# Performance work log

Hardware: AMD Instinct MI355X
Metric: run time of the kernel (lower is better)

## Reference

```python
import jax, jax.numpy as jnp
import numpy as np

SR = 3            # search_range
K = 5             # template_sz
S = 2 * SR + 1    # search window size (7)
KSZ = 5           # bilateral kernel size
SIG_S = 1.5       # bilateral spatial sigma
SIG_I = 0.05      # bilateral intensity sigma


def _patches(x, k, pad):
    # x: (B,C,H,W) -> (B, C*k*k, H', W'); channel order (C, kh, kw) matches torch unfold
    return jax.lax.conv_general_dilated_patches(x, (k, k), (1, 1), pad)


def _binomial(x):
    # separable [1 2 1]/4 with replicate padding
    xp = jnp.pad(x, ((0, 0), (0, 0), (1, 1), (0, 0)), mode='edge')
    v = (xp[:, :, :-2, :] + 2.0 * x + xp[:, :, 2:, :]) / 4.0
    vp = jnp.pad(v, ((0, 0), (0, 0), (0, 0), (1, 1)), mode='edge')
    return (vp[:, :, :, :-2] + 2.0 * v + vp[:, :, :, 2:]) / 4.0


def _gradient(f):
    fp = jnp.pad(f, ((0, 0), (0, 0), (1, 1), (1, 1)), mode='edge')
    fy = (fp[:, :, 2:, 1:-1] - fp[:, :, :-2, 1:-1]) / 2.0
    fx = (fp[:, :, 1:-1, 2:] - fp[:, :, 1:-1, :-2]) / 2.0
    return fy, fx


def _templates(img):
    # (B,1,H,W) -> (B,H,W,1,K*K)  per-pixel KxK patch (zero SAME padding)
    p = _patches(img, K, [(K // 2, K // 2)] * 2)      # (B,K*K,H,W)
    return jnp.transpose(p, (0, 2, 3, 1))[:, :, :, None, :]


def _search_windows(img):
    # (B,1,H,W) -> (B,H,W,S*S,K*K): KxK templates at every displacement in SxS window
    B, _, H, W = img.shape
    xp = jnp.pad(img, ((0, 0), (0, 0), (SR, SR), (SR, SR)))      # zero pad by max_sr
    p1 = _patches(xp, K, [(K // 2, K // 2)] * 2)                  # (B,K*K,H+2SR,W+2SR)
    p2 = _patches(p1, S, 'VALID')                                 # (B,K*K*S*S,H,W)
    p2 = p2.reshape(B, K * K, S, S, H, W)
    return jnp.transpose(p2, (0, 4, 5, 2, 3, 1)).reshape(B, H, W, S * S, K * K)


def _spiral_rank():
    # rank of each flat (S*S) displacement in a center-out spiral traversal
    sz = S
    order = np.zeros(sz * sz, np.int32)
    j = i = 0
    rank = 0
    order[(j + SR) * sz + (i + SR)] = rank
    rank += 1
    dirs = [(0, 1), (1, 0), (0, -1), (-1, 0)]
    d, step = 0, 1
    while rank < sz * sz:
        for _ in range(2):
            dj, di = dirs[d % 4]
            for _ in range(step):
                j += dj
                i += di
                if abs(j) <= SR and abs(i) <= SR and rank < sz * sz:
                    order[(j + SR) * sz + (i + SR)] = rank
                    rank += 1
            d += 1
        step += 1
    return jnp.asarray(order)


def _subpixel(f_t, g_t, f_img):
    # f_t, g_t: (B,H,W,1,K*K) in 0..255; f_img: (B,1,H,W) float in [0,1]
    f = f_t / 255.0
    g = g_t / 255.0
    dfy_img, dfx_img = _gradient(f_img)
    dfy = _templates(dfy_img)
    dfx = _templates(dfx_img)
    pm = np.zeros((K, K), np.float32)
    pm[0, :] = pm[-1, :] = pm[:, 0] = pm[:, -1] = 1.0   # border ring mask
    pred = jnp.asarray(pm.reshape(-1))
    rs = lambda x: jnp.sum(x, axis=-1, keepdims=True)
    a = rs(dfx * dfx * pred)
    b = rs(dfx * dfy * pred)
    d = rs(dfy * dfy * pred)
    z = g - f
    p = rs(z * dfx * pred)
    q = rs(z * dfy * pred)
    det = a * d - b * b
    u = d * p - b * q
    v = a * q - b * p
    sub = jnp.concatenate([v, u], axis=-1)              # (B,H,W,1,2) (y,x)
    det_bad = det <= 1e-7
    sub = sub / jnp.where(det_bad, 1.0, det)            # safe divide; masked anyway
    sub = jnp.where(det_bad | (jnp.abs(sub) >= 1.0), 0.0, sub)
    return jnp.transpose(sub[:, :, :, 0, :], (0, 3, 1, 2))   # (B,2,H,W)


def _median3(x):
    # 3x3 median with replicate (SYMMETRIC) padding
    B, C, H, W = x.shape
    xp = jnp.pad(x, ((0, 0), (0, 0), (1, 1), (1, 1)), mode='edge')
    p = _patches(xp, 3, 'VALID').reshape(B, C, 9, H, W)
    return jnp.sort(p, axis=2)[:, :, 4]


def _bilateral(t, vec):
    # t: (B,1,H,W) guide; vec: (B,2,H,W) flow
    B, _, H, W = t.shape
    k2 = KSZ * KSZ
    kernel = -1.0 / (2.0 * SIG_S ** 2) * jnp.ones((k2,), jnp.float32)
    sii = 1.0 / (2.0 * SIG_I ** 2)
    cp = jnp.transpose(t, (0, 2, 3, 1))[:, :, :, None, :]                # (B,H,W,1,1)
    ck = jnp.transpose(_patches(t, KSZ, [(KSZ // 2, KSZ // 2)] * 2).reshape(B, 1, k2, H, W), (0, 3, 4, 2, 1))  # (B,H,W,k2,1)
    idiff = jnp.sum((cp - ck) ** 2, axis=-1)                             # (B,H,W,k2)
    coeff = jnp.clip(1.0 - jnp.abs(kernel - idiff * sii), 0.0, 1.0)[..., None]
    vb = jnp.transpose(_patches(vec, KSZ, [(KSZ // 2, KSZ // 2)] * 2).reshape(B, 2, k2, H, W), (0, 3, 4, 2, 1))  # (B,H,W,k2,2)
    out = jnp.sum(vb * coeff, axis=-2) / jnp.sum(coeff, axis=-2)
    return jnp.transpose(out, (0, 3, 1, 2))


def setup_inputs() -> dict:
    key = jax.random.key(0)
    k1, k2 = jax.random.split(key)
    H = W = 256
    f_img = jax.random.uniform(k1, (1, 1, H, W), jnp.float32)
    g_img = jax.random.uniform(k2, (1, 1, H, W), jnp.float32)
    return {'f_img': f_img, 'g_img': g_img}


def reference(f_img, g_img):
    fb = _binomial(f_img)
    gb = _binomial(g_img)
    # quantize to uint8-valued floats (matches _cast float->uint8)
    fq = jnp.clip(jnp.round(fb * 255.0), 0.0, 255.0)
    gq = jnp.clip(jnp.round(gb * 255.0), 0.0, 255.0)
    w1 = _search_windows(fq)                 # (B,H,W,S*S,K*K)
    w2 = _templates(gq)                      # (B,H,W,1,K*K)
    cost = jnp.sum(jnp.abs(w1 - w2), axis=-1).astype(jnp.int32)   # (B,H,W,S*S)
    rank = _spiral_rank()
    score = cost * 64 + rank                 # lexicographic (cost, spiral rank); rank < 64
    idx = jnp.argmin(score, axis=-1)         # (B,H,W) spiral-centered argmin
    rng = jnp.arange(-SR, SR + 1, dtype=jnp.float32)
    jj, ii = jnp.meshgrid(rng, rng, indexing='ij')
    vecLUT = -jnp.stack([jj, ii], axis=-1).reshape(-1, 2)
    vector = jnp.transpose(vecLUT[idx], (0, 3, 1, 2))             # (B,2,H,W)
    min_t = jnp.take_along_axis(w1, idx[:, :, :, None, None], axis=3)  # (B,H,W,1,K*K)
    sub = _subpixel(min_t, w2, fb)
    flow = vector + sub
    flow = _median3(flow)
    flow = _bilateral(fb, flow)
    return flow
```

## Files before the change

kernel.cpp:

```cpp
#include <hip/hip_runtime.h>
#include <math.h>

#define H 256
#define W 256
#define TS 16

#if __has_builtin(__builtin_amdgcn_alignbyte)
__device__ __forceinline__ unsigned align_b(unsigned hi, unsigned lo, int sh) {
    return __builtin_amdgcn_alignbyte(hi, lo, sh);
}
#else
__device__ __forceinline__ unsigned align_b(unsigned hi, unsigned lo, int sh) {
    unsigned d;
    asm("v_alignbyte_b32 %0, %1, %2, %3" : "=v"(d) : "v"(hi), "v"(lo), "v"(sh));
    return d;
}
#endif

#if __has_builtin(__builtin_amdgcn_sad_u8)
__device__ __forceinline__ unsigned sad_u8(unsigned a, unsigned b, unsigned acc) {
    return __builtin_amdgcn_sad_u8(a, b, acc);
}
#else
__device__ __forceinline__ unsigned sad_u8(unsigned a, unsigned b, unsigned acc) {
    unsigned d;
    asm("v_sad_u8 %0, %1, %2, %3" : "=v"(d) : "v"(a), "v"(b), "v"(acc));
    return d;
}
#endif

__global__ void k_binq(const float* __restrict__ f, const float* __restrict__ g,
                       float* __restrict__ fb,
                       unsigned char* __restrict__ fq, unsigned char* __restrict__ gq) {
    int x = blockIdx.x * blockDim.x + threadIdx.x;
    int y = blockIdx.y * blockDim.y + threadIdx.y;
    if (x >= W || y >= H) return;
    int ym = max(y - 1, 0), yp = min(y + 1, H - 1);
    int xm = max(x - 1, 0), xp = min(x + 1, W - 1);

    float fvm = (f[ym*W+xm] + 2.0f*f[y*W+xm] + f[yp*W+xm]) * 0.25f;
    float fv0 = (f[ym*W+x ] + 2.0f*f[y*W+x ] + f[yp*W+x ]) * 0.25f;
    float fvp = (f[ym*W+xp] + 2.0f*f[y*W+xp] + f[yp*W+xp]) * 0.25f;
    float fbv = (fvm + 2.0f*fv0 + fvp) * 0.25f;

    float gvm = (g[ym*W+xm] + 2.0f*g[y*W+xm] + g[yp*W+xm]) * 0.25f;
    float gv0 = (g[ym*W+x ] + 2.0f*g[y*W+x ] + g[yp*W+x ]) * 0.25f;
    float gvp = (g[ym*W+xp] + 2.0f*g[y*W+xp] + g[yp*W+xp]) * 0.25f;
    float gbv = (gvm + 2.0f*gv0 + gvp) * 0.25f;

    fb[y*W+x] = fbv;
    fq[y*W+x] = (unsigned char)fminf(fmaxf(rintf(fbv * 255.0f), 0.0f), 255.0f);
    gq[y*W+x] = (unsigned char)fminf(fmaxf(rintf(gbv * 255.0f), 0.0f), 255.0f);
}

__global__ void __launch_bounds__(256)
k_search(const unsigned char* __restrict__ fq, const unsigned char* __restrict__ gq,
         const float* __restrict__ fb, float* __restrict__ flow) {
    __shared__ unsigned sfq[26 * 7];
    __shared__ unsigned sgq[20 * 5];
    __shared__ float    sfb[22 * 22];

    int tx = threadIdx.x, ty = threadIdx.y;
    int bx0 = blockIdx.x * TS, by0 = blockIdx.y * TS;
    int tid = ty * TS + tx;

    unsigned char* sfq_b = (unsigned char*)sfq;
    unsigned char* sgq_b = (unsigned char*)sgq;

    for (int i = tid; i < 26 * 28; i += 256) {
        int r = i / 28, c = i % 28;
        int gy = by0 + r - 5, gx = bx0 + c - 5;
        sfq_b[i] = (gy >= 0 && gy < H && gx >= 0 && gx < W) ? fq[gy*W+gx] : 0;
    }
    for (int i = tid; i < 20 * 20; i += 256) {
        int r = i / 20, c = i % 20;
        int gy = by0 + r - 2, gx = bx0 + c - 2;
        sgq_b[r * 20 + c] = (gy >= 0 && gy < H && gx >= 0 && gx < W) ? gq[gy*W+gx] : 0;
    }
    for (int i = tid; i < 22 * 22; i += 256) {
        int r = i / 22, c = i % 22;
        int gy = min(max(by0 + r - 3, 0), H - 1);
        int gx = min(max(bx0 + c - 3, 0), W - 1);
        sfb[i] = fb[gy*W+gx];
    }
    __syncthreads();

    int x = bx0 + tx, y = by0 + ty;
    int base = tx >> 2, a = tx & 3;

    unsigned w0[11], w1[11], w2[11];
    #pragma unroll
    for (int r = 0; r < 11; r++) {
        const unsigned* row = &sfq[(ty + r) * 7 + base];
        unsigned d0 = row[0], d1 = row[1], d2 = row[2], d3 = row[3];
        w0[r] = align_b(d1, d0, a);
        w1[r] = align_b(d2, d1, a);
        w2[r] = align_b(d3, d2, a);
    }

    unsigned gt_lo[5], gt_hi[5];
    #pragma unroll
    for (int r = 0; r < 5; r++) {
        const unsigned* row = &sgq[(ty + r) * 5 + base];
        unsigned d0 = row[0], d1 = row[1];
        gt_lo[r] = align_b(d1, d0, a);
        gt_hi[r] = (d1 >> (8 * a)) & 0xFFu;
    }

    const unsigned RANKC[49] = {
        42,43,44,45,46,47,48,
        41,20,21,22,23,24,25,
        40,19, 6, 7, 8, 9,26,
        39,18, 5, 0, 1,10,27,
        38,17, 4, 3, 2,11,28,
        37,16,15,14,13,12,29,
        36,35,34,33,32,31,30
    };

    unsigned best = 0xFFFFFFFFu;
    int bestd = 0;
    #pragma unroll
    for (int si = 0; si < 7; si++) {
        unsigned fd[11], f5[11];
        #pragma unroll
        for (int r = 0; r < 11; r++) {
            fd[r] = (si < 4) ? align_b(w1[r], w0[r], si) : align_b(w2[r], w1[r], si - 4);
            f5[r] = (si < 4) ? ((w1[r] >> (8 * si)) & 0xFFu)
                             : ((w2[r] >> (8 * (si - 4))) & 0xFFu);
        }
        #pragma unroll
        for (int sj = 0; sj < 7; sj++) {
            unsigned acc0 = 0, acc1 = 0;
            #pragma unroll
            for (int kh = 0; kh < 5; kh++) {
                acc0 = sad_u8(fd[sj + kh], gt_lo[kh], acc0);
                acc1 = sad_u8(f5[sj + kh], gt_hi[kh], acc1);
            }
            unsigned score = ((acc0 + acc1) << 6) + RANKC[sj * 7 + si];
            if (score < best) { best = score; bestd = sj * 7 + si; }
        }
    }
    int dy = bestd / 7 - 3, dx = bestd % 7 - 3;

    float aA = 0.f, bB = 0.f, dD = 0.f, pP = 0.f, qQ = 0.f;
    #pragma unroll
    for (int kh = 0; kh < 5; kh++) {
        #pragma unroll
        for (int kw = 0; kw < 5; kw++) {
            if (kh != 0 && kh != 4 && kw != 0 && kw != 4) continue;
            int yy = y + kh - 2, xx = x + kw - 2;
            if (yy < 0 || yy >= H || xx < 0 || xx >= W) continue;
            int ry = ty + kh + 1, rx = tx + kw + 1;
            float gxv = (sfb[ry*22 + rx+1] - sfb[ry*22 + rx-1]) * 0.5f;
            float gyv = (sfb[(ry+1)*22 + rx] - sfb[(ry-1)*22 + rx]) * 0.5f;
            float fv = (float)sfq_b[(ty + dy + kh + 3) * 28 + (tx + dx + kw + 3)] * (1.0f/255.0f);
            float gv = (float)((kw < 4) ? ((gt_lo[kh] >> (8*kw)) & 0xFFu) : gt_hi[kh]) * (1.0f/255.0f);
            float z = gv - fv;
            aA += gxv * gxv;
            bB += gxv * gyv;
            dD += gyv * gyv;
            pP += z * gxv;
            qQ += z * gyv;
        }
    }
    float det = aA * dD - bB * bB;
    float u = dD * pP - bB * qQ;
    float v = aA * qQ - bB * pP;
    float suby = 0.f, subx = 0.f;
    if (det > 1e-7f) {
        suby = v / det;
        subx = u / det;
        if (fabsf(suby) >= 1.0f) suby = 0.f;
        if (fabsf(subx) >= 1.0f) subx = 0.f;
    }
    flow[y*W + x]       = (float)(-dy) + suby;
    flow[H*W + y*W + x] = (float)(-dx) + subx;
}

__global__ void __launch_bounds__(256)
k_medbil(const float* __restrict__ flow1, const float* __restrict__ fb,
         float* __restrict__ out) {
    __shared__ float sfl[2][22 * 22];
    __shared__ float smed[2][20 * 20];
    __shared__ float sfbt[20 * 20];

    int tx = threadIdx.x, ty = threadIdx.y;
    int bx0 = blockIdx.x * TS, by0 = blockIdx.y * TS;
    int tid = ty * TS + tx;

    for (int i = tid; i < 2 * 22 * 22; i += 256) {
        int c = i / 484, rem = i % 484;
        int r = rem / 22, col = rem % 22;
        int qy = min(max(by0 + r - 3, 0), H - 1);
        int qx = min(max(bx0 + col - 3, 0), W - 1);
        sfl[c][rem] = flow1[c*H*W + qy*W + qx];
    }
    for (int i = tid; i < 20 * 20; i += 256) {
        int r = i / 20, col = i % 20;
        int yy = by0 + r - 2, xx = bx0 + col - 2;
        sfbt[i] = (yy >= 0 && yy < H && xx >= 0 && xx < W) ? fb[yy*W+xx] : 0.0f;
    }
    __syncthreads();

    for (int i = tid; i < 2 * 20 * 20; i += 256) {
        int c = i / 400, rem = i % 400;
        int r = rem / 20, col = rem % 20;
        int py = by0 + r - 2, px = bx0 + col - 2;
        float m = 0.0f;
        if (py >= 0 && py < H && px >= 0 && px < W) {
            float v[9];
            int n = 0;
            #pragma unroll
            for (int j = 0; j < 3; j++)
                #pragma unroll
                for (int ii = 0; ii < 3; ii++)
                    v[n++] = sfl[c][(r + j) * 22 + (col + ii)];
#define MSWAP(A, B) { float t_ = fminf(v[A], v[B]); v[B] = fmaxf(v[A], v[B]); v[A] = t_; }
            MSWAP(1,2); MSWAP(4,5); MSWAP(7,8);
            MSWAP(0,1); MSWAP(3,4); MSWAP(6,7);
            MSWAP(1,2); MSWAP(4,5); MSWAP(7,8);
            MSWAP(0,3); MSWAP(5,8); MSWAP(4,7);
            MSWAP(3,6); MSWAP(1,4); MSWAP(2,5);
            MSWAP(4,7); MSWAP(4,2); MSWAP(6,4);
            MSWAP(4,2);
#undef MSWAP
            m = v[4];
        }
        smed[c][rem] = m;
    }
    __syncthreads();

    int x = bx0 + tx, y = by0 + ty;
    const float kern = -0.22222222222222221f;
    const float sii  = 200.0f;
    float cp = sfbt[(ty + 2) * 20 + (tx + 2)];
    float sc = 0.f, sy = 0.f, sx = 0.f;
    #pragma unroll
    for (int j = 0; j < 5; j++) {
        #pragma unroll
        for (int i = 0; i < 5; i++) {
            int s = (ty + j) * 20 + (tx + i);
            float ck = sfbt[s];
            float df = cp - ck;
            float coeff = 1.0f - fabsf(kern - df * df * sii);
            coeff = fminf(fmaxf(coeff, 0.0f), 1.0f);
            sc += coeff;
            sy += coeff * smed[0][s];
            sx += coeff * smed[1][s];
        }
    }
    out[y*W + x]       = sy / sc;
    out[H*W + y*W + x] = sx / sc;
}

extern "C" void kernel_launch(void* const* d_in, const int* in_sizes, int n_in,
                              void* d_out, int out_size, void* d_ws, size_t ws_size,
                              hipStream_t stream) {
    const float* f = (const float*)d_in[0];
    const float* g = (const float*)d_in[1];
    float* out = (float*)d_out;

    char* ws = (char*)d_ws;
    float*         fb    = (float*)(ws);
    unsigned char* fq    = (unsigned char*)(ws + 262144);
    unsigned char* gq    = (unsigned char*)(ws + 327680);
    float*         flow1 = (float*)(ws + 393216);

    dim3 blk(TS, TS);
    dim3 grd(W / TS, H / TS);
    k_binq  <<<grd, blk, 0, stream>>>(f, g, fb, fq, gq);
    k_search<<<grd, blk, 0, stream>>>(fq, gq, fb, flow1);
    k_medbil<<<grd, blk, 0, stream>>>(flow1, fb, out);
}
```

Baseline: 67.98 us.

## Fuse three stages into one cooperative kernel with grid-wide syncs

Merges the blur/quantize, block-matching search and median+bilateral kernels into one cooperative kernel separated by grid.sync barriers, with a shared-memory union reused across phases. The aim is to remove two kernel launch gaps. The 256-block grid must be co-resident, and grid-wide barriers plus a cooperative launch add their own overhead.

```diff
diff --git a/kernel.cpp b/kernel.cpp
--- a/kernel.cpp
+++ b/kernel.cpp
@@ -1,5 +1,8 @@
 #include <hip/hip_runtime.h>
+#include <hip/hip_cooperative_groups.h>
 #include <math.h>
+
+namespace cg = cooperative_groups;
 
 #define H 256
 #define W 256
@@ -29,228 +32,231 @@
 }
 #endif
 
-__global__ void k_binq(const float* __restrict__ f, const float* __restrict__ g,
-                       float* __restrict__ fb,
-                       unsigned char* __restrict__ fq, unsigned char* __restrict__ gq) {
-    int x = blockIdx.x * blockDim.x + threadIdx.x;
-    int y = blockIdx.y * blockDim.y + threadIdx.y;
-    if (x >= W || y >= H) return;
-    int ym = max(y - 1, 0), yp = min(y + 1, H - 1);
-    int xm = max(x - 1, 0), xp = min(x + 1, W - 1);
-
-    float fvm = (f[ym*W+xm] + 2.0f*f[y*W+xm] + f[yp*W+xm]) * 0.25f;
-    float fv0 = (f[ym*W+x ] + 2.0f*f[y*W+x ] + f[yp*W+x ]) * 0.25f;
-    float fvp = (f[ym*W+xp] + 2.0f*f[y*W+xp] + f[yp*W+xp]) * 0.25f;
-    float fbv = (fvm + 2.0f*fv0 + fvp) * 0.25f;
-
-    float gvm = (g[ym*W+xm] + 2.0f*g[y*W+xm] + g[yp*W+xm]) * 0.25f;
-    float gv0 = (g[ym*W+x ] + 2.0f*g[y*W+x ] + g[yp*W+x ]) * 0.25f;
-    float gvp = (g[ym*W+xp] + 2.0f*g[y*W+xp] + g[yp*W+xp]) * 0.25f;
-    float gbv = (gvm + 2.0f*gv0 + gvp) * 0.25f;
-
-    fb[y*W+x] = fbv;
-    fq[y*W+x] = (unsigned char)fminf(fmaxf(rintf(fbv * 255.0f), 0.0f), 255.0f);
-    gq[y*W+x] = (unsigned char)fminf(fmaxf(rintf(gbv * 255.0f), 0.0f), 255.0f);
-}
-
 __global__ void __launch_bounds__(256)
-k_search(const unsigned char* __restrict__ fq, const unsigned char* __restrict__ gq,
-         const float* __restrict__ fb, float* __restrict__ flow) {
-    __shared__ unsigned sfq[26 * 7];
-    __shared__ unsigned sgq[20 * 5];
-    __shared__ float    sfb[22 * 22];
+k_fused(const float* __restrict__ f, const float* __restrict__ g,
+        float* __restrict__ fb, unsigned char* __restrict__ fq,
+        unsigned char* __restrict__ gq, float* __restrict__ flow1,
+        float* __restrict__ out) {
+    __shared__ union {
+        struct {
+            unsigned sfq[26 * 7];
+            unsigned sgq[20 * 5];
+            float    sfb[22 * 22];
+        } p2;
+        struct {
+            float sfl[2 * 22 * 22];
+            float smed[2 * 20 * 20];
+            float sfbt[20 * 20];
+        } p3;
+    } sh;
+
+    cg::grid_group grid = cg::this_grid();
 
     int tx = threadIdx.x, ty = threadIdx.y;
     int bx0 = blockIdx.x * TS, by0 = blockIdx.y * TS;
     int tid = ty * TS + tx;
-
-    unsigned char* sfq_b = (unsigned char*)sfq;
-    unsigned char* sgq_b = (unsigned char*)sgq;
-
-    for (int i = tid; i < 26 * 28; i += 256) {
-        int r = i / 28, c = i % 28;
-        int gy = by0 + r - 5, gx = bx0 + c - 5;
-        sfq_b[i] = (gy >= 0 && gy < H && gx >= 0 && gx < W) ? fq[gy*W+gx] : 0;
+    int x = bx0 + tx, y = by0 + ty;
+
+    {
+        int ym = max(y - 1, 0), yp = min(y + 1, H - 1);
+        int xm = max(x - 1, 0), xp = min(x + 1, W - 1);
+
+        float fvm = (f[ym*W+xm] + 2.0f*f[y*W+xm] + f[yp*W+xm]) * 0.25f;
+        float fv0 = (f[ym*W+x ] + 2.0f*f[y*W+x ] + f[yp*W+x ]) * 0.25f;
+        float fvp = (f[ym*W+xp] + 2.0f*f[y*W+xp] + f[yp*W+xp]) * 0.25f;
+        float fbv = (fvm + 2.0f*fv0 + fvp) * 0.25f;
+
+        float gvm = (g[ym*W+xm] + 2.0f*g[y*W+xm] + g[yp*W+xm]) * 0.25f;
+        float gv0 = (g[ym*W+x ] + 2.0f*g[y*W+x ] + g[yp*W+x ]) * 0.25f;
+        float gvp = (g[ym*W+xp] + 2.0f*g[y*W+xp] + g[yp*W+xp]) * 0.25f;
+        float gbv = (gvm + 2.0f*gv0 + gvp) * 0.25f;
+
+        fb[y*W+x] = fbv;
+        fq[y*W+x] = (unsigned char)fminf(fmaxf(rintf(fbv * 255.0f), 0.0f), 255.0f);
+        gq[y*W+x] = (unsigned char)fminf(fmaxf(rintf(gbv * 255.0f), 0.0f), 255.0f);
     }
-    for (int i = tid; i < 20 * 20; i += 256) {
-        int r = i / 20, c = i % 20;
-        int gy = by0 + r - 2, gx = bx0 + c - 2;
-        sgq_b[r * 20 + c] = (gy >= 0 && gy < H && gx >= 0 && gx < W) ? gq[gy*W+gx] : 0;
+    __threadfence();
+    grid.sync();
+
+    {
+        unsigned char* sfq_b = (unsigned char*)sh.p2.sfq;
+        unsigned char* sgq_b = (unsigned char*)sh.p2.sgq;
+
+        for (int i = tid; i < 26 * 28; i += 256) {
+            int r = i / 28, c = i % 28;
+            int gy = by0 + r - 5, gx = bx0 + c - 5;
+            sfq_b[i] = (gy >= 0 && gy < H && gx >= 0 && gx < W) ? fq[gy*W+gx] : 0;
+        }
+        for (int i = tid; i < 20 * 20; i += 256) {
+            int r = i / 20, c = i % 20;
+            int gy = by0 + r - 2, gx = bx0 + c - 2;
+            sgq_b[r * 20 + c] = (gy >= 0 && gy < H && gx >= 0 && gx < W) ? gq[gy*W+gx] : 0;
+        }
+        for (int i = tid; i < 22 * 22; i += 256) {
+            int r = i / 22, c = i % 22;
+            int gy = min(max(by0 + r - 3, 0), H - 1);
+            int gx = min(max(bx0 + c - 3, 0), W - 1);
+            sh.p2.sfb[i] = fb[gy*W+gx];
+        }
+        __syncthreads();
+
+        int base = tx >> 2, a = tx & 3;
+
+        unsigned w0[11], w1[11], w2[11];
+        #pragma unroll
+        for (int r = 0; r < 11; r++) {
+            const unsigned* row = &sh.p2.sfq[(ty + r) * 7 + base];
+            unsigned d0 = row[0], d1 = row[1], d2 = row[2], d3 = row[3];
+            w0[r] = align_b(d1, d0, a);
+            w1[r] = align_b(d2, d1, a);
+            w2[r] = align_b(d3, d2, a);
+        }
+
+        unsigned gt_lo[5], gt_hi[5];
+        #pragma unroll
+        for (int r = 0; r < 5; r++) {
+            const unsigned* row = &sh.p2.sgq[(ty + r) * 5 + base];
+            unsigned d0 = row[0], d1 = row[1];
+            gt_lo[r] = align_b(d1, d0, a);
+            gt_hi[r] = (d1 >> (8 * a)) & 0xFFu;
+        }
+
+        const unsigned RANKC[49] = {
+            42,43,44,45,46,47,48,
+            41,20,21,22,23,24,25,
+            40,19, 6, 7, 8, 9,26,
+            39,18, 5, 0, 1,10,27,
+            38,17, 4, 3, 2,11,28,
+            37,16,15,14,13,12,29,
+            36,35,34,33,32,31,30
+        };
+
+        unsigned best = 0xFFFFFFFFu;
+        int bestd = 0;
+        #pragma unroll
+        for (int si = 0; si < 7; si++) {
+            unsigned fd[11], f5[11];
+            #pragma unroll
+            for (int r = 0; r < 11; r++) {
+                fd[r] = (si < 4) ? align_b(w1[r], w0[r], si) : align_b(w2[r], w1[r], si - 4);
+                f5[r] = (si < 4) ? ((w1[r] >> (8 * si)) & 0xFFu)
+                                 : ((w2[r] >> (8 * (si - 4))) & 0xFFu);
+            }
+            #pragma unroll
+            for (int sj = 0; sj < 7; sj++) {
+                unsigned acc0 = 0, acc1 = 0;
+                #pragma unroll
+                for (int kh = 0; kh < 5; kh++) {
+                    acc0 = sad_u8(fd[sj + kh], gt_lo[kh], acc0);
+                    acc1 = sad_u8(f5[sj + kh], gt_hi[kh], acc1);
+                }
+                unsigned score = ((acc0 + acc1) << 6) + RANKC[sj * 7 + si];
+                if (score < best) { best = score; bestd = sj * 7 + si; }
+            }
+        }
+        int dy = bestd / 7 - 3, dx = bestd % 7 - 3;
+
+        float aA = 0.f, bB = 0.f, dD = 0.f, pP = 0.f, qQ = 0.f;
+        #pragma unroll
+        for (int kh = 0; kh < 5; kh++) {
+            #pragma unroll
+            for (int kw = 0; kw < 5; kw++) {
+                if (kh != 0 && kh != 4 && kw != 0 && kw != 4) continue;
+                int yy = y + kh - 2, xx = x + kw - 2;
+                if (yy < 0 || yy >= H || xx < 0 || xx >= W) continue;
+                int ry = ty + kh + 1, rx = tx + kw + 1;
+                float gxv = (sh.p2.sfb[ry*22 + rx+1] - sh.p2.sfb[ry*22 + rx-1]) * 0.5f;
+                float gyv = (sh.p2.sfb[(ry+1)*22 + rx] - sh.p2.sfb[(ry-1)*22 + rx]) * 0.5f;
+                float fv = (float)sfq_b[(ty + dy + kh + 3) * 28 + (tx + dx + kw + 3)] * (1.0f/255.0f);
+                float gv = (float)((kw < 4) ? ((gt_lo[kh] >> (8*kw)) & 0xFFu) : gt_hi[kh]) * (1.0f/255.0f);
+                float z = gv - fv;
+                aA += gxv * gxv;
+                bB += gxv * gyv;
+                dD += gyv * gyv;
+                pP += z * gxv;
+                qQ += z * gyv;
+            }
+        }
+        float det = aA * dD - bB * bB;
+        float u = dD * pP - bB * qQ;
+        float v = aA * qQ - bB * pP;
+        float suby = 0.f, subx = 0.f;
+        if (det > 1e-7f) {
+            suby = v / det;
+            subx = u / det;
+            if (fabsf(suby) >= 1.0f) suby = 0.f;
+            if (fabsf(subx) >= 1.0f) subx = 0.f;
+        }
+        flow1[y*W + x]       = (float)(-dy) + suby;
+        flow1[H*W + y*W + x] = (float)(-dx) + subx;
     }
-    for (int i = tid; i < 22 * 22; i += 256) {
-        int r = i / 22, c = i % 22;
-        int gy = min(max(by0 + r - 3, 0), H - 1);
-        int gx = min(max(bx0 + c - 3, 0), W - 1);
-        sfb[i] = fb[gy*W+gx];
+    __threadfence();
+    grid.sync();
+
+    {
+        for (int i = tid; i < 2 * 22 * 22; i += 256) {
+            int c = i / 484, rem = i % 484;
+            int r = rem / 22, col = rem % 22;
+            int qy = min(max(by0 + r - 3, 0), H - 1);
+            int qx = min(max(bx0 + col - 3, 0), W - 1);
+            sh.p3.sfl[c * 484 + rem] = flow1[c*H*W + qy*W + qx];
+        }
+        for (int i = tid; i < 20 * 20; i += 256) {
+            int r = i / 20, col = i % 20;
+            int yy = by0 + r - 2, xx = bx0 + col - 2;
+            sh.p3.sfbt[i] = (yy >= 0 && yy < H && xx >= 0 && xx < W) ? fb[yy*W+xx] : 0.0f;
+        }
+        __syncthreads();
+
+        for (int i = tid; i < 2 * 20 * 20; i += 256) {
+            int c = i / 400, rem = i % 400;
+            int r = rem / 20, col = rem % 20;
+            int py = by0 + r - 2, px = bx0 + col - 2;
+            float m = 0.0f;
+            if (py >= 0 && py < H && px >= 0 && px < W) {
+                float v[9];
+                int n = 0;
+                #pragma unroll
+                for (int j = 0; j < 3; j++)
+                    #pragma unroll
+                    for (int ii = 0; ii < 3; ii++)
+                        v[n++] = sh.p3.sfl[c * 484 + (r + j) * 22 + (col + ii)];
+#define MSWAP(A, B) { float t_ = fminf(v[A], v[B]); v[B] = fmaxf(v[A], v[B]); v[A] = t_; }
+                MSWAP(1,2); MSWAP(4,5); MSWAP(7,8);
+                MSWAP(0,1); MSWAP(3,4); MSWAP(6,7);
+                MSWAP(1,2); MSWAP(4,5); MSWAP(7,8);
+                MSWAP(0,3); MSWAP(5,8); MSWAP(4,7);
+                MSWAP(3,6); MSWAP(1,4); MSWAP(2,5);
+                MSWAP(4,7); MSWAP(4,2); MSWAP(6,4);
+                MSWAP(4,2);
+#undef MSWAP
+                m = v[4];
+            }
+            sh.p3.smed[c * 400 + rem] = m;
+        }
+        __syncthreads();
+
+        const float kern = -0.22222222222222221f;
+        const float sii  = 200.0f;
+        float cp = sh.p3.sfbt[(ty + 2) * 20 + (tx + 2)];
+        float sc = 0.f, sy = 0.f, sx = 0.f;
+        #pragma unroll
+        for (int j = 0; j < 5; j++) {
+            #pragma unroll
+            for (int i = 0; i < 5; i++) {
+                int s = (ty + j) * 20 + (tx + i);
+                float ck = sh.p3.sfbt[s];
+                float df = cp - ck;
+                float coeff = 1.0f - fabsf(kern - df * df * sii);
+                coeff = fminf(fmaxf(coeff, 0.0f), 1.0f);
+                sc += coeff;
+                sy += coeff * sh.p3.smed[0 * 400 + s];
+                sx += coeff * sh.p3.smed[1 * 400 + s];
+            }
+        }
+        out[y*W + x]       = sy / sc;
+        out[H*W + y*W + x] = sx / sc;
     }
-    __syncthreads();
-
-    int x = bx0 + tx, y = by0 + ty;
-    int base = tx >> 2, a = tx & 3;
-
-    unsigned w0[11], w1[11], w2[11];
-    #pragma unroll
-    for (int r = 0; r < 11; r++) {
-        const unsigned* row = &sfq[(ty + r) * 7 + base];
-        unsigned d0 = row[0], d1 = row[1], d2 = row[2], d3 = row[3];
-        w0[r] = align_b(d1, d0, a);
-        w1[r] = align_b(d2, d1, a);
-        w2[r] = align_b(d3, d2, a);
-    }
-
-    unsigned gt_lo[5], gt_hi[5];
-    #pragma unroll
-    for (int r = 0; r < 5; r++) {
-        const unsigned* row = &sgq[(ty + r) * 5 + base];
-        unsigned d0 = row[0], d1 = row[1];
-        gt_lo[r] = align_b(d1, d0, a);
-        gt_hi[r] = (d1 >> (8 * a)) & 0xFFu;
-    }
-
-    const unsigned RANKC[49] = {
-        42,43,44,45,46,47,48,
-        41,20,21,22,23,24,25,
-        40,19, 6, 7, 8, 9,26,
-        39,18, 5, 0, 1,10,27,
-        38,17, 4, 3, 2,11,28,
-        37,16,15,14,13,12,29,
-        36,35,34,33,32,31,30
-    };
-
-    unsigned best = 0xFFFFFFFFu;
-    int bestd = 0;
-    #pragma unroll
-    for (int si = 0; si < 7; si++) {
-        unsigned fd[11], f5[11];
-        #pragma unroll
-        for (int r = 0; r < 11; r++) {
-            fd[r] = (si < 4) ? align_b(w1[r], w0[r], si) : align_b(w2[r], w1[r], si - 4);
-            f5[r] = (si < 4) ? ((w1[r] >> (8 * si)) & 0xFFu)
-                             : ((w2[r] >> (8 * (si - 4))) & 0xFFu);
-        }
-        #pragma unroll
-        for (int sj = 0; sj < 7; sj++) {
-            unsigned acc0 = 0, acc1 = 0;
-            #pragma unroll
-            for (int kh = 0; kh < 5; kh++) {
-                acc0 = sad_u8(fd[sj + kh], gt_lo[kh], acc0);
-                acc1 = sad_u8(f5[sj + kh], gt_hi[kh], acc1);
-            }
-            unsigned score = ((acc0 + acc1) << 6) + RANKC[sj * 7 + si];
-            if (score < best) { best = score; bestd = sj * 7 + si; }
-        }
-    }
-    int dy = bestd / 7 - 3, dx = bestd % 7 - 3;
-
-    float aA = 0.f, bB = 0.f, dD = 0.f, pP = 0.f, qQ = 0.f;
-    #pragma unroll
-    for (int kh = 0; kh < 5; kh++) {
-        #pragma unroll
-        for (int kw = 0; kw < 5; kw++) {
-            if (kh != 0 && kh != 4 && kw != 0 && kw != 4) continue;
-            int yy = y + kh - 2, xx = x + kw - 2;
-            if (yy < 0 || yy >= H || xx < 0 || xx >= W) continue;
-            int ry = ty + kh + 1, rx = tx + kw + 1;
-            float gxv = (sfb[ry*22 + rx+1] - sfb[ry*22 + rx-1]) * 0.5f;
-            float gyv = (sfb[(ry+1)*22 + rx] - sfb[(ry-1)*22 + rx]) * 0.5f;
-            float fv = (float)sfq_b[(ty + dy + kh + 3) * 28 + (tx + dx + kw + 3)] * (1.0f/255.0f);
-            float gv = (float)((kw < 4) ? ((gt_lo[kh] >> (8*kw)) & 0xFFu) : gt_hi[kh]) * (1.0f/255.0f);
-            float z = gv - fv;
-            aA += gxv * gxv;
-            bB += gxv * gyv;
-            dD += gyv * gyv;
-            pP += z * gxv;
-            qQ += z * gyv;
-        }
-    }
-    float det = aA * dD - bB * bB;
-    float u = dD * pP - bB * qQ;
-    float v = aA * qQ - bB * pP;
-    float suby = 0.f, subx = 0.f;
-    if (det > 1e-7f) {
-        suby = v / det;
-        subx = u / det;
-        if (fabsf(suby) >= 1.0f) suby = 0.f;
-        if (fabsf(subx) >= 1.0f) subx = 0.f;
-    }
-    flow[y*W + x]       = (float)(-dy) + suby;
-    flow[H*W + y*W + x] = (float)(-dx) + subx;
-}
-
-__global__ void __launch_bounds__(256)
-k_medbil(const float* __restrict__ flow1, const float* __restrict__ fb,
-         float* __restrict__ out) {
-    __shared__ float sfl[2][22 * 22];
-    __shared__ float smed[2][20 * 20];
-    __shared__ float sfbt[20 * 20];
-
-    int tx = threadIdx.x, ty = threadIdx.y;
-    int bx0 = blockIdx.x * TS, by0 = blockIdx.y * TS;
-    int tid = ty * TS + tx;
-
-    for (int i = tid; i < 2 * 22 * 22; i += 256) {
-        int c = i / 484, rem = i % 484;
-        int r = rem / 22, col = rem % 22;
-        int qy = min(max(by0 + r - 3, 0), H - 1);
-        int qx = min(max(bx0 + col - 3, 0), W - 1);
-        sfl[c][rem] = flow1[c*H*W + qy*W + qx];
-    }
-    for (int i = tid; i < 20 * 20; i += 256) {
-        int r = i / 20, col = i % 20;
-        int yy = by0 + r - 2, xx = bx0 + col - 2;
-        sfbt[i] = (yy >= 0 && yy < H && xx >= 0 && xx < W) ? fb[yy*W+xx] : 0.0f;
-    }
-    __syncthreads();
-
-    for (int i = tid; i < 2 * 20 * 20; i += 256) {
-        int c = i / 400, rem = i % 400;
-        int r = rem / 20, col = rem % 20;
-        int py = by0 + r - 2, px = bx0 + col - 2;
-        float m = 0.0f;
-        if (py >= 0 && py < H && px >= 0 && px < W) {
-            float v[9];
-            int n = 0;
-            #pragma unroll
-            for (int j = 0; j < 3; j++)
-                #pragma unroll
-                for (int ii = 0; ii < 3; ii++)
-                    v[n++] = sfl[c][(r + j) * 22 + (col + ii)];
-#define MSWAP(A, B) { float t_ = fminf(v[A], v[B]); v[B] = fmaxf(v[A], v[B]); v[A] = t_; }
-            MSWAP(1,2); MSWAP(4,5); MSWAP(7,8);
-            MSWAP(0,1); MSWAP(3,4); MSWAP(6,7);
-            MSWAP(1,2); MSWAP(4,5); MSWAP(7,8);
-            MSWAP(0,3); MSWAP(5,8); MSWAP(4,7);
-            MSWAP(3,6); MSWAP(1,4); MSWAP(2,5);
-            MSWAP(4,7); MSWAP(4,2); MSWAP(6,4);
-            MSWAP(4,2);
-#undef MSWAP
-            m = v[4];
-        }
-        smed[c][rem] = m;
-    }
-    __syncthreads();
-
-    int x = bx0 + tx, y = by0 + ty;
-    const float kern = -0.22222222222222221f;
-    const float sii  = 200.0f;
-    float cp = sfbt[(ty + 2) * 20 + (tx + 2)];
-    float sc = 0.f, sy = 0.f, sx = 0.f;
-    #pragma unroll
-    for (int j = 0; j < 5; j++) {
-        #pragma unroll
-        for (int i = 0; i < 5; i++) {
-            int s = (ty + j) * 20 + (tx + i);
-            float ck = sfbt[s];
-            float df = cp - ck;
-            float coeff = 1.0f - fabsf(kern - df * df * sii);
-            coeff = fminf(fmaxf(coeff, 0.0f), 1.0f);
-            sc += coeff;
-            sy += coeff * smed[0][s];
-            sx += coeff * smed[1][s];
-        }
-    }
-    out[y*W + x]       = sy / sc;
-    out[H*W + y*W + x] = sx / sc;
 }
 
 extern "C" void kernel_launch(void* const* d_in, const int* in_sizes, int n_in,
@@ -266,9 +272,8 @@
     unsigned char* gq    = (unsigned char*)(ws + 327680);
     float*         flow1 = (float*)(ws + 393216);
 
-    dim3 blk(TS, TS);
-    dim3 grd(W / TS, H / TS);
-    k_binq  <<<grd, blk, 0, stream>>>(f, g, fb, fq, gq);
-    k_search<<<grd, blk, 0, stream>>>(fq, gq, fb, flow1);
-    k_medbil<<<grd, blk, 0, stream>>>(flow1, fb, out);
-}
+    void* args[] = { (void*)&f, (void*)&g, (void*)&fb, (void*)&fq,
+                     (void*)&gq, (void*)&flow1, (void*)&out };
+    hipLaunchCooperativeKernel((void*)k_fused, dim3(W / TS, H / TS), dim3(TS, TS),
+                               args, 0, stream);
+}
```

Result: slower. 172.1 us (+153.1%).
